# Kernel tuning notes

Hardware: AMD Instinct MI355X
Metric: run time of the kernel (lower is better)

Reference implementation:

```python
import jax, jax.numpy as jnp
import numpy as np

B, T, D_MODEL = 2, 2048, 2048
N_HEADS, N_KV, HEAD_DIM = 16, 8, 128
ROPE_BASE = 10000.0
LAMBDA_INIT = 0.2  # 0.8 - 0.6*exp(-0.3*0), layer_depth=0


def rms_norm(x):
    eps = jnp.finfo(x.dtype).eps
    return x * jax.lax.rsqrt(jnp.mean(x * x, axis=-1, keepdims=True) + eps)


def rope_cos_sin(seq_len, dim):
    inv_freq = 1.0 / (ROPE_BASE ** (np.arange(0, dim, 2, dtype=np.float32) / dim))
    t = np.arange(seq_len, dtype=np.float32)
    freqs = np.outer(t, inv_freq)  # [T, dim/2]
    # original caches cos/sin in bfloat16
    cos = jnp.asarray(np.cos(freqs)).astype(jnp.bfloat16).astype(jnp.float32)
    sin = jnp.asarray(np.sin(freqs)).astype(jnp.bfloat16).astype(jnp.float32)
    return cos[None, :, None, :], sin[None, :, None, :]


def apply_rotary(x, cos, sin):
    d = x.shape[-1] // 2
    x1, x2 = x[..., :d], x[..., d:]
    return jnp.concatenate([x1 * cos + x2 * sin, -x1 * sin + x2 * cos], axis=-1)


def causal_attn(q, k, v):
    # q: [B,T,H,Dq], k: [B,S,H,Dq], v: [B,S,H,Dv]
    scale = 1.0 / np.sqrt(q.shape[-1]).astype(np.float32)
    s = jnp.einsum('bthd,bshd->bhts', q, k) * scale
    mask = jnp.tril(jnp.ones((q.shape[1], k.shape[1]), dtype=bool))
    s = jnp.where(mask, s, -jnp.inf)
    p = jax.nn.softmax(s, axis=-1)
    return jnp.einsum('bhts,bshe->bthe', p, v)


def diff_attention(x, Wq, Wk, Wv, lambda_q1, lambda_k1, lambda_q2, lambda_k2, softmax_scaler):
    b, t, _ = x.shape
    q = (x @ Wq.T).reshape(b, t, N_HEADS, HEAD_DIM)
    k = (x @ Wk.T).reshape(b, t, N_KV, HEAD_DIM)
    v = (x @ Wv.T).reshape(b, t, N_KV // 2, 2 * HEAD_DIM)
    cos, sin = rope_cos_sin(t, HEAD_DIM)
    q, k = rms_norm(q), rms_norm(k)
    q, k = apply_rotary(q, cos, sin), apply_rotary(k, cos, sin)
    k = k.reshape(b, t, 2, N_KV // 2, HEAD_DIM)
    k1, k2 = k[:, :, 0], k[:, :, 1]
    # scalable softmax: q *= scaler_h * log(position)
    pos = jnp.arange(1, t + 1, dtype=jnp.float32).reshape(1, t, 1, 1)
    q = softmax_scaler.reshape(1, 1, -1, 1) * jnp.log(pos) * q
    q = q.reshape(b, t, 2, N_HEADS // 2, HEAD_DIM)
    q1, q2 = q[:, :, 0], q[:, :, 1]
    rep = N_HEADS // N_KV  # GQA repeat
    k1 = jnp.repeat(k1, rep, axis=2)
    k2 = jnp.repeat(k2, rep, axis=2)
    vr = jnp.repeat(v, rep, axis=2)
    y1 = causal_attn(q1, k1, vr)
    y2 = causal_attn(q2, k2, vr)
    lam1 = jnp.exp(jnp.sum(lambda_q1 * lambda_k1))
    lam2 = jnp.exp(jnp.sum(lambda_q2 * lambda_k2))
    lam = lam1 - lam2 + LAMBDA_INIT
    return y1 - lam * y2  # [B,T,N_HEADS//2, 2*HEAD_DIM]


def setup_inputs() -> dict:
    key = jax.random.key(0)
    ks = jax.random.split(key, 8)
    return {
        'x': jax.random.normal(ks[0], (B, T, D_MODEL), dtype=jnp.float32),
        'Wq': jax.random.normal(ks[1], (N_HEADS * HEAD_DIM, D_MODEL), dtype=jnp.float32) * 0.02,
        'Wk': jax.random.normal(ks[2], (N_KV * HEAD_DIM, D_MODEL), dtype=jnp.float32) * 0.02,
        'Wv': jax.random.normal(ks[3], (N_KV * HEAD_DIM, D_MODEL), dtype=jnp.float32) * 0.02,
        'lambda_q1': jax.random.normal(ks[4], (HEAD_DIM // 2,), dtype=jnp.float32) * 0.1,
        'lambda_k1': jax.random.normal(ks[5], (HEAD_DIM // 2,), dtype=jnp.float32) * 0.1,
        'lambda_q2': jax.random.normal(ks[6], (HEAD_DIM // 2,), dtype=jnp.float32) * 0.1,
        'lambda_k2': jax.random.normal(ks[7], (HEAD_DIM // 2,), dtype=jnp.float32) * 0.1,
        'softmax_scaler': jnp.ones((N_HEADS,), dtype=jnp.float32),
    }


def reference(x, Wq, Wk, Wv, lambda_q1, lambda_k1, lambda_q2, lambda_k2, softmax_scaler):
    return diff_attention(x, Wq, Wk, Wv, lambda_q1, lambda_k1, lambda_q2, lambda_k2, softmax_scaler)
```

## Files before the change

### kernel.cpp

```cpp
#include <hip/hip_runtime.h>

#define T_SEQ 2048
#define DMODEL 2048
#define BSZ 2
#define MROWS (BSZ * T_SEQ)
#define NQKV 4096
#define NEG_BIG (-1e30f)

typedef __attribute__((ext_vector_type(8))) _Float16 half8;
typedef __attribute__((ext_vector_type(4))) _Float16 half4;
typedef __attribute__((ext_vector_type(4))) float f32x4;

typedef const __attribute__((address_space(1))) unsigned int* gas_ptr;
typedef __attribute__((address_space(3))) unsigned int* las_ptr;
#define GLD16(g, l) __builtin_amdgcn_global_load_lds((gas_ptr)(g), (las_ptr)(l), 16, 0, 0)

__device__ __forceinline__ unsigned short f2bf(float f) {
  unsigned u = __float_as_uint(f);
  unsigned r = (u + 0x7fffu + ((u >> 16) & 1u)) >> 16;
  return (unsigned short)r;
}
__device__ __forceinline__ float bf2f(unsigned short h) {
  return __uint_as_float(((unsigned)h) << 16);
}

__global__ __launch_bounds__(256) void prep(const float* __restrict__ x,
                                            const float* __restrict__ Wq,
                                            const float* __restrict__ Wk,
                                            const float* __restrict__ Wv,
                                            _Float16* __restrict__ xh,
                                            _Float16* __restrict__ wh,
                                            float* __restrict__ cosT,
                                            float* __restrict__ sinT) {
  int bid = blockIdx.x;
  if (bid < 8192) {
    size_t o = ((size_t)(bid & 4095) * 256 + threadIdx.x) * 8;
    const float* src;
    _Float16* dst;
    if (bid < 4096) {
      src = x + o;
      dst = xh + o;
    } else {
      int row = (int)(o >> 11), col = (int)(o & 2047);
      src = ((row < 2048) ? (Wq + (size_t)row * 2048)
            : (row < 3072) ? (Wk + (size_t)(row - 2048) * 2048)
                           : (Wv + (size_t)(row - 3072) * 2048)) + col;
      dst = wh + o;
    }
    float4 v0 = *(const float4*)(src);
    float4 v1 = *(const float4*)(src + 4);
    half8 r;
    r[0] = (_Float16)v0.x; r[1] = (_Float16)v0.y; r[2] = (_Float16)v0.z; r[3] = (_Float16)v0.w;
    r[4] = (_Float16)v1.x; r[5] = (_Float16)v1.y; r[6] = (_Float16)v1.z; r[7] = (_Float16)v1.w;
    *(half8*)(dst) = r;
  } else {
    int t = bid - 8192;
    int i = threadIdx.x;
    if (i < 64) {
      float inv = (float)pow(10000.0, -((double)(2 * i)) / 128.0);
      float fr = (float)t * inv;
      cosT[t * 64 + i] = bf2f(f2bf(cosf(fr)));
      sinT[t * 64 + i] = bf2f(f2bf(sinf(fr)));
    }
  }
}

__global__ __launch_bounds__(256) void gemm_nt(const _Float16* __restrict__ A,
                                               const _Float16* __restrict__ Bw,
                                               _Float16* __restrict__ C) {
  const int K = DMODEL, N = NQKV;
  __shared__ __align__(16) char As[2][128 * 128];
  __shared__ __align__(16) char Bs[2][128 * 128];
  int tid = threadIdx.x;
  int lane = tid & 63, w = tid >> 6;
  int wm = w >> 1, wn = w & 1;
  int l15 = lane & 15, quad = lane >> 4;
  int bm = blockIdx.y, bn = blockIdx.x;

  const char* Aab = (const char*)(A + (size_t)(bm * 128) * K);
  const char* Bab = (const char*)(Bw + (size_t)(bn * 128) * K);
  int srow = lane >> 3;
  int scol = ((lane & 7) ^ srow) << 4;

  auto stage = [&](int t) {
    int buf = t & 1;
    size_t kb = (size_t)t << 7;
#pragma unroll
    for (int g = 0; g < 4; g++) {
      int row = w * 32 + g * 8 + srow;
      GLD16(Aab + (size_t)row * (K * 2) + kb + scol, &As[buf][w * 4096 + g * 1024]);
    }
#pragma unroll
    for (int g = 0; g < 4; g++) {
      int row = w * 32 + g * 8 + srow;
      GLD16(Bab + (size_t)row * (K * 2) + kb + scol, &Bs[buf][w * 4096 + g * 1024]);
    }
  };

  f32x4 acc[4][4];
#pragma unroll
  for (int i = 0; i < 4; i++)
#pragma unroll
    for (int j = 0; j < 4; j++) acc[i][j] = (f32x4){0.f, 0.f, 0.f, 0.f};

  stage(0);
  for (int t = 0; t < 32; t++) {
    if (t < 31) {
      stage(t + 1);
      asm volatile("s_waitcnt vmcnt(8)" ::: "memory");
    } else {
      asm volatile("s_waitcnt vmcnt(0)" ::: "memory");
    }
    __builtin_amdgcn_s_barrier();
    __builtin_amdgcn_sched_barrier(0);

    const char* ab = As[t & 1];
    const char* bb = Bs[t & 1];
#pragma unroll
    for (int kc = 0; kc < 2; kc++) {
      half8 af[4], bfr[4];
#pragma unroll
      for (int i = 0; i < 4; i++) {
        int row = wm * 64 + i * 16 + l15;
        af[i] = *(const half8*)(ab + row * 128 + ((kc * 64 + quad * 16) ^ ((row & 7) << 4)));
      }
#pragma unroll
      for (int j = 0; j < 4; j++) {
        int row = wn * 64 + j * 16 + l15;
        bfr[j] = *(const half8*)(bb + row * 128 + ((kc * 64 + quad * 16) ^ ((row & 7) << 4)));
      }
#pragma unroll
      for (int i = 0; i < 4; i++)
#pragma unroll
        for (int j = 0; j < 4; j++)
          acc[i][j] = __builtin_amdgcn_mfma_f32_16x16x32_f16(af[i], bfr[j], acc[i][j], 0, 0, 0);
    }

    asm volatile("s_waitcnt lgkmcnt(0)" ::: "memory");
    __builtin_amdgcn_s_barrier();
    __builtin_amdgcn_sched_barrier(0);
  }

#pragma unroll
  for (int i = 0; i < 4; i++)
#pragma unroll
    for (int j = 0; j < 4; j++)
#pragma unroll
      for (int r = 0; r < 4; r++) {
        int row = bm * 128 + wm * 64 + i * 16 + quad * 4 + r;
        int col = bn * 128 + wn * 64 + j * 16 + l15;
        C[(size_t)row * N + col] = (_Float16)acc[i][j][r];
      }
}

__global__ __launch_bounds__(256) void mid(_Float16* __restrict__ qkv,
                                           const float* __restrict__ cosT,
                                           const float* __restrict__ sinT,
                                           _Float16* __restrict__ kp,
                                           _Float16* __restrict__ vt) {
  __shared__ _Float16 tile[32][33];
  int bid = blockIdx.x;
  if (bid < 6144) {
    int tid = threadIdx.x, lane = tid & 63, w = tid >> 6;
    int h = bid >> 8;
    int tkn = (bid & 255) * 16 + w * 4 + (lane >> 4);
    int b = tkn >> 11, t = tkn & 2047;
    int l15 = lane & 15;
    int col0 = (h < 16) ? (h * 128) : (2048 + (h - 16) * 128);
    size_t base = (size_t)tkn * NQKV + col0 + l15 * 8;

    half8 v = *(const half8*)(qkv + base);
    float xf[8];
    float ss = 0.f;
#pragma unroll
    for (int j = 0; j < 8; j++) { xf[j] = (float)v[j]; ss += xf[j] * xf[j]; }
    ss += __shfl_xor(ss, 1, 64);
    ss += __shfl_xor(ss, 2, 64);
    ss += __shfl_xor(ss, 4, 64);
    ss += __shfl_xor(ss, 8, 64);
    float rn = rsqrtf(ss * (1.0f / 128.0f) + 1.1920929e-7f);

    const float* cb = cosT + t * 64 + (lane & 7) * 8;
    const float* sb = sinT + t * 64 + (lane & 7) * 8;
    float4 c0 = *(const float4*)cb, c1 = *(const float4*)(cb + 4);
    float4 s0 = *(const float4*)sb, s1 = *(const float4*)(sb + 4);
    float cc[8] = {c0.x, c0.y, c0.z, c0.w, c1.x, c1.y, c1.z, c1.w};
    float sn[8] = {s0.x, s0.y, s0.z, s0.w, s1.x, s1.y, s1.z, s1.w};
    float sgn = (lane & 8) ? -1.f : 1.f;

    half8 o;
#pragma unroll
    for (int j = 0; j < 8; j++) {
      float xn = xf[j] * rn;
      float xp = __shfl_xor(xn, 8, 64);
      o[j] = (_Float16)(xn * cc[j] + sgn * xp * sn[j]);
    }
    if (h < 16)
      *(half8*)(qkv + base) = o;
    else
      *(half8*)(kp + (((size_t)(b * 8 + (h - 16))) * T_SEQ + t) * 128 + l15 * 8) = o;
  } else {
    int tb = bid - 6144;
    int t0 = (tb & 63) * 32, d0 = ((tb >> 6) & 7) * 32;
    int bz = tb >> 9;
    int b = bz >> 2, vh = bz & 3;
    int tx = threadIdx.x & 31, ty = threadIdx.x >> 5;
#pragma unroll
    for (int i = 0; i < 4; i++) {
      int t = t0 + ty + i * 8;
      tile[ty + i * 8][tx] = qkv[((size_t)(b * T_SEQ + t)) * NQKV + 3072 + vh * 256 + d0 + tx];
    }
    __syncthreads();
#pragma unroll
    for (int i = 0; i < 4; i++) {
      int d = d0 + ty + i * 8;
      vt[(((size_t)(b * 4 + vh)) * 256 + d) * T_SEQ + t0 + tx] = tile[tx][ty + i * 8];
    }
  }
}

__global__ __launch_bounds__(256) void attn(const _Float16* __restrict__ qkv,
                                            const _Float16* __restrict__ kp,
                                            const _Float16* __restrict__ vt,
                                            const float* __restrict__ scaler,
                                            float* __restrict__ y1out,
                                            _Float16* __restrict__ y2out) {
  __shared__ __align__(16) char Ks[2][64 * 256];
  __shared__ __align__(16) char Vs[2][128 * 128];
  __shared__ _Float16 Pt[4 * 16 * 72];

  int tid = threadIdx.x, lane = tid & 63, w = tid >> 6;
  int l15 = lane & 15, quad = lane >> 4;
  int bx = blockIdx.x, hh = blockIdx.y, z = blockIdx.z;
  int b = z >> 1, br = z & 1;
  int qh = br * 8 + hh;
  int kh = br * 4 + (hh >> 1);
  int vh = hh >> 1;

  const char* kbase_b = (const char*)(kp + ((size_t)(b * 8 + kh)) * T_SEQ * 128);
  const char* vbase_b = (const char*)(vt + ((size_t)(b * 4 + vh)) * 256 * T_SEQ);
  _Float16* pw = &Pt[w * 16 * 72];
  float sc = scaler[qh] * 0.08838834764831844f;

  int krow_l = lane >> 4;
  int kpc    = (lane & 15) << 4;
  int vrow_l = lane >> 3;
  int vpc    = (lane & 7) << 4;

  auto stageK = [&](int kt1) {
    int ksr = kt1 * 64;
    char* dstb = Ks[kt1 & 1];
#pragma unroll
    for (int c2 = 0; c2 < 4; c2++) {
      int cc = w * 4 + c2;
      int row = cc * 4 + krow_l;
      const char* src = kbase_b + (((size_t)(ksr + row)) << 8) + (kpc ^ ((row & 7) << 4));
      GLD16(src, dstb + (cc << 10));
    }
  };
  auto stageV = [&](int kt1) {
    int ksb = kt1 * 128;
#pragma unroll
    for (int h = 0; h < 2; h++)
#pragma unroll
      for (int c2 = 0; c2 < 4; c2++) {
        int cc = w * 4 + c2;
        int d = h * 128 + cc * 8 + vrow_l;
        const char* src = vbase_b + (size_t)d * (T_SEQ * 2) + ksb + (vpc ^ (vrow_l << 4));
        GLD16(src, Vs[h] + (cc << 10));
      }
  };

  for (int half = 0; half < 2; half++) {
    int qt = half ? (31 - bx) : bx;
    int t0 = qt * 64;
    int tg = t0 + w * 16 + l15;

    const _Float16* qbase = qkv + ((size_t)(b * T_SEQ + tg)) * NQKV + qh * 128;
    half8 qf[4];
#pragma unroll
    for (int kc = 0; kc < 4; kc++)
      qf[kc] = *(const half8*)(qbase + kc * 32 + quad * 8);

    stageK(0);
    stageV(0);
    __builtin_amdgcn_sched_barrier(0);

    float mrow = NEG_BIG, lrow = 0.f;
    float rowscale = sc * logf((float)(tg + 1)) * 1.44269504f;
    f32x4 acc[16];
#pragma unroll
    for (int nb = 0; nb < 16; nb++) acc[nb] = (f32x4){0.f, 0.f, 0.f, 0.f};

    for (int kt = 0; kt <= qt; kt++) {
      int ks = kt * 64;
      bool notlast = (kt < qt);

      asm volatile("s_waitcnt vmcnt(8)" ::: "memory");
      __builtin_amdgcn_s_barrier();
      __builtin_amdgcn_sched_barrier(0);
      if (notlast) stageK(kt + 1);

      const char* kbuf = Ks[kt & 1];
      f32x4 sv[4];
#pragma unroll
      for (int j = 0; j < 4; j++) {
        int row = j * 16 + l15;
        int sw = (row & 7) << 4;
        const char* kr = kbuf + (row << 8);
        half8 kf0 = *(const half8*)(kr + (((quad << 4) + 0) ^ sw));
        half8 kf1 = *(const half8*)(kr + (((quad << 4) + 64) ^ sw));
        half8 kf2 = *(const half8*)(kr + (((quad << 4) + 128) ^ sw));
        half8 kf3 = *(const half8*)(kr + (((quad << 4) + 192) ^ sw));
        f32x4 a = (f32x4){0.f, 0.f, 0.f, 0.f};
        a = __builtin_amdgcn_mfma_f32_16x16x32_f16(kf0, qf[0], a, 0, 0, 0);
        a = __builtin_amdgcn_mfma_f32_16x16x32_f16(kf1, qf[1], a, 0, 0, 0);
        a = __builtin_amdgcn_mfma_f32_16x16x32_f16(kf2, qf[2], a, 0, 0, 0);
        a = __builtin_amdgcn_mfma_f32_16x16x32_f16(kf3, qf[3], a, 0, 0, 0);
        sv[j] = a;
      }

      bool diag = (kt == qt);
      float s_r[16];
      float mx = NEG_BIG;
#pragma unroll
      for (int j = 0; j < 4; j++)
#pragma unroll
        for (int r = 0; r < 4; r++) {
          float s = sv[j][r] * rowscale;
          if (diag) {
            int kg = ks + j * 16 + quad * 4 + r;
            if (kg > tg) s = NEG_BIG;
          }
          s_r[j * 4 + r] = s;
          mx = fmaxf(mx, s);
        }
      mx = fmaxf(mx, __shfl_xor(mx, 16, 64));
      mx = fmaxf(mx, __shfl_xor(mx, 32, 64));
      float mnew = fmaxf(mrow, mx);
      float alpha = __builtin_amdgcn_exp2f(mrow - mnew);
      float p[16];
      float rs = 0.f;
#pragma unroll
      for (int i = 0; i < 16; i++) {
        p[i] = __builtin_amdgcn_exp2f(s_r[i] - mnew);
        rs += p[i];
      }
      rs += __shfl_xor(rs, 16, 64);
      rs += __shfl_xor(rs, 32, 64);
      lrow = lrow * alpha + rs;
      mrow = mnew;
#pragma unroll
      for (int nb = 0; nb < 16; nb++)
#pragma unroll
        for (int r = 0; r < 4; r++) acc[nb][r] *= alpha;

#pragma unroll
      for (int j = 0; j < 4; j++) {
        half4 pk;
        pk[0] = (_Float16)p[j * 4 + 0];
        pk[1] = (_Float16)p[j * 4 + 1];
        pk[2] = (_Float16)p[j * 4 + 2];
        pk[3] = (_Float16)p[j * 4 + 3];
        *(half4*)&pw[l15 * 72 + j * 16 + quad * 4] = pk;
      }
      half8 pf0 = *(const half8*)&pw[l15 * 72 + quad * 8];
      half8 pf1 = *(const half8*)&pw[l15 * 72 + 32 + quad * 8];

      if (notlast)
        asm volatile("s_waitcnt vmcnt(4)" ::: "memory");
      else
        asm volatile("s_waitcnt vmcnt(0)" ::: "memory");
      __builtin_amdgcn_s_barrier();
      __builtin_amdgcn_sched_barrier(0);

#pragma unroll
      for (int h = 0; h < 2; h++) {
#pragma unroll
        for (int nbl = 0; nbl < 8; nbl++) {
          int row = nbl * 16 + l15;
          int sw = (row & 7) << 4;
          const char* vr = Vs[h] + (row << 7);
          half8 vf0 = *(const half8*)(vr + (((quad << 4) + 0) ^ sw));
          half8 vf1 = *(const half8*)(vr + (((quad << 4) + 64) ^ sw));
          int nb = h * 8 + nbl;
          acc[nb] = __builtin_amdgcn_mfma_f32_16x16x32_f16(vf0, pf0, acc[nb], 0, 0, 0);
          acc[nb] = __builtin_amdgcn_mfma_f32_16x16x32_f16(vf1, pf1, acc[nb], 0, 0, 0);
        }
      }

      asm volatile("s_waitcnt lgkmcnt(0)" ::: "memory");
      __builtin_amdgcn_s_barrier();
      __builtin_amdgcn_sched_barrier(0);
      if (notlast) stageV(kt + 1);
    }

    float linv = 1.0f / lrow;
    size_t base = ((size_t)(b * T_SEQ + tg)) * 2048 + hh * 256 + quad * 4;
    if (br) {
#pragma unroll
      for (int nb = 0; nb < 16; nb++) {
        half4 hv;
        hv[0] = (_Float16)(acc[nb][0] * linv);
        hv[1] = (_Float16)(acc[nb][1] * linv);
        hv[2] = (_Float16)(acc[nb][2] * linv);
        hv[3] = (_Float16)(acc[nb][3] * linv);
        *(half4*)(y2out + base + nb * 16) = hv;
      }
    } else {
#pragma unroll
      for (int nb = 0; nb < 16; nb++) {
        float4 fv;
        fv.x = acc[nb][0] * linv;
        fv.y = acc[nb][1] * linv;
        fv.z = acc[nb][2] * linv;
        fv.w = acc[nb][3] * linv;
        *(float4*)(y1out + base + nb * 16) = fv;
      }
    }
  }
}

__global__ __launch_bounds__(256) void combine(float* __restrict__ out,
                                               const _Float16* __restrict__ y2,
                                               const float* __restrict__ lq1,
                                               const float* __restrict__ lk1,
                                               const float* __restrict__ lq2,
                                               const float* __restrict__ lk2) {
  int lane = threadIdx.x & 63;
  float a = lq1[lane] * lk1[lane];
  float bb = lq2[lane] * lk2[lane];
#pragma unroll
  for (int m = 1; m < 64; m <<= 1) {
    a += __shfl_xor(a, m, 64);
    bb += __shfl_xor(bb, m, 64);
  }
  float lam = expf(a) - expf(bb) + 0.2f;

  size_t o = ((size_t)blockIdx.x * 256 + threadIdx.x) * 8;
  half8 yv = *(const half8*)(y2 + o);
  float4 a0 = *(float4*)(out + o);
  float4 a1 = *(float4*)(out + o + 4);
  a0.x -= lam * (float)yv[0];
  a0.y -= lam * (float)yv[1];
  a0.z -= lam * (float)yv[2];
  a0.w -= lam * (float)yv[3];
  a1.x -= lam * (float)yv[4];
  a1.y -= lam * (float)yv[5];
  a1.z -= lam * (float)yv[6];
  a1.w -= lam * (float)yv[7];
  *(float4*)(out + o) = a0;
  *(float4*)(out + o + 4) = a1;
}

extern "C" void kernel_launch(void* const* d_in, const int* in_sizes, int n_in,
                              void* d_out, int out_size, void* d_ws, size_t ws_size,
                              hipStream_t stream) {
  const float* x   = (const float*)d_in[0];
  const float* Wq  = (const float*)d_in[1];
  const float* Wk  = (const float*)d_in[2];
  const float* Wv  = (const float*)d_in[3];
  const float* lq1 = (const float*)d_in[4];
  const float* lk1 = (const float*)d_in[5];
  const float* lq2 = (const float*)d_in[6];
  const float* lk2 = (const float*)d_in[7];
  const float* scaler = (const float*)d_in[8];
  float* out = (float*)d_out;

  char* W = (char*)d_ws;
  _Float16* xh   = (_Float16*)(W + 0);
  _Float16* wh   = (_Float16*)(W + 16777216);
  _Float16* qkvh = (_Float16*)(W + 33554432);
  _Float16* kph  = (_Float16*)(W + 0);
  _Float16* vtb  = (_Float16*)(W + 8388608);
  _Float16* y2h  = (_Float16*)(W + 16777216);
  float* cosT    = out;
  float* sinT    = out + 131072;

  prep<<<10240, 256, 0, stream>>>(x, Wq, Wk, Wv, xh, wh, cosT, sinT);
  gemm_nt<<<dim3(NQKV / 128, MROWS / 128), 256, 0, stream>>>(xh, wh, qkvh);
  mid<<<10240, 256, 0, stream>>>(qkvh, cosT, sinT, kph, vtb);
  attn<<<dim3(16, 8, BSZ * 2), 256, 0, stream>>>(qkvh, kph, vtb, scaler, out, y2h);
  combine<<<4096, 256, 0, stream>>>(out, y2h, lq1, lk1, lq2, lk2);
}
```

Baseline: 313.5 us.

## Enlarge QKV GEMM to 256x256 tiles with 8 waves and interleaved scheduling

The QKV projection GEMM moves from 128x128 tiles with 4 waves to 256x256 tiles with 8 waves. Each wave now computes a 128x64 sub-tile, with LDS reads interleaved against MFMA batches under barriers and s_setprio hints, and the next k-tile prefetch is issued mid-iteration. This raises operand reuse per LDS byte and cuts global traffic. The cost is 128KB of LDS, more accumulator registers, and only 256 blocks, which is about one wave of work on 256 CUs.

After: 314.3 us. No clear change (+0.3%).

```diff
diff --git a/kernel.cpp b/kernel.cpp
--- a/kernel.cpp
+++ b/kernel.cpp
@@ -65,91 +65,124 @@
   }
 }
 
-__global__ __launch_bounds__(256) void gemm_nt(const _Float16* __restrict__ A,
+__global__ __launch_bounds__(512) void gemm_nt(const _Float16* __restrict__ A,
                                                const _Float16* __restrict__ Bw,
                                                _Float16* __restrict__ C) {
   const int K = DMODEL, N = NQKV;
-  __shared__ __align__(16) char As[2][128 * 128];
-  __shared__ __align__(16) char Bs[2][128 * 128];
+  __shared__ __align__(16) char As[2][2][16384];
+  __shared__ __align__(16) char Bs[2][2][16384];
   int tid = threadIdx.x;
   int lane = tid & 63, w = tid >> 6;
-  int wm = w >> 1, wn = w & 1;
+  int wr = w >> 2, wc = w & 3;
+  int cb = wc & 1, bh = wc >> 1;
   int l15 = lane & 15, quad = lane >> 4;
   int bm = blockIdx.y, bn = blockIdx.x;
 
-  const char* Aab = (const char*)(A + (size_t)(bm * 128) * K);
-  const char* Bab = (const char*)(Bw + (size_t)(bn * 128) * K);
-  int srow = lane >> 3;
-  int scol = ((lane & 7) ^ srow) << 4;
+  const char* Aab = (const char*)(A + (size_t)(bm * 256) * K);
+  const char* Bab = (const char*)(Bw + (size_t)(bn * 256) * K);
+  int scol = ((lane & 7) ^ (lane >> 3)) << 4;
 
   auto stage = [&](int t) {
-    int buf = t & 1;
-    size_t kb = (size_t)t << 7;
-#pragma unroll
-    for (int g = 0; g < 4; g++) {
-      int row = w * 32 + g * 8 + srow;
-      GLD16(Aab + (size_t)row * (K * 2) + kb + scol, &As[buf][w * 4096 + g * 1024]);
-    }
-#pragma unroll
-    for (int g = 0; g < 4; g++) {
-      int row = w * 32 + g * 8 + srow;
-      GLD16(Bab + (size_t)row * (K * 2) + kb + scol, &Bs[buf][w * 4096 + g * 1024]);
+    int bt = t & 1;
+    int kb = t * 128;
+#pragma unroll
+    for (int g = 0; g < 8; g++) {
+      int mtx = g >> 2;
+      int h   = (g >> 1) & 1;
+      int j   = g & 1;
+      int row = h * 128 + w * 16 + j * 8 + (lane >> 3);
+      const char* src = (mtx ? Bab : Aab) + (size_t)row * (K * 2) + kb + scol;
+      char* dst = (mtx ? &Bs[bt][h][0] : &As[bt][h][0]) + (w * 16 + j * 8) * 128;
+      GLD16(src, dst);
     }
   };
 
-  f32x4 acc[4][4];
-#pragma unroll
-  for (int i = 0; i < 4; i++)
+  f32x4 acc[8][4];
+#pragma unroll
+  for (int i = 0; i < 8; i++)
 #pragma unroll
     for (int j = 0; j < 4; j++) acc[i][j] = (f32x4){0.f, 0.f, 0.f, 0.f};
 
   stage(0);
+  asm volatile("s_waitcnt vmcnt(0)" ::: "memory");
+  __builtin_amdgcn_s_barrier();
+  __builtin_amdgcn_sched_barrier(0);
+
   for (int t = 0; t < 32; t++) {
-    if (t < 31) {
-      stage(t + 1);
-      asm volatile("s_waitcnt vmcnt(8)" ::: "memory");
-    } else {
-      asm volatile("s_waitcnt vmcnt(0)" ::: "memory");
-    }
-    __builtin_amdgcn_s_barrier();
-    __builtin_amdgcn_sched_barrier(0);
-
-    const char* ab = As[t & 1];
-    const char* bb = Bs[t & 1];
-#pragma unroll
-    for (int kc = 0; kc < 2; kc++) {
-      half8 af[4], bfr[4];
-#pragma unroll
-      for (int i = 0; i < 4; i++) {
-        int row = wm * 64 + i * 16 + l15;
-        af[i] = *(const half8*)(ab + row * 128 + ((kc * 64 + quad * 16) ^ ((row & 7) << 4)));
-      }
-#pragma unroll
-      for (int j = 0; j < 4; j++) {
-        int row = wn * 64 + j * 16 + l15;
-        bfr[j] = *(const half8*)(bb + row * 128 + ((kc * 64 + quad * 16) ^ ((row & 7) << 4)));
-      }
-#pragma unroll
-      for (int i = 0; i < 4; i++)
-#pragma unroll
-        for (int j = 0; j < 4; j++)
-          acc[i][j] = __builtin_amdgcn_mfma_f32_16x16x32_f16(af[i], bfr[j], acc[i][j], 0, 0, 0);
-    }
-
-    asm volatile("s_waitcnt lgkmcnt(0)" ::: "memory");
-    __builtin_amdgcn_s_barrier();
-    __builtin_amdgcn_sched_barrier(0);
-  }
-
-#pragma unroll
-  for (int i = 0; i < 4; i++)
-#pragma unroll
-    for (int j = 0; j < 4; j++)
+    const char* Ahb = &As[t & 1][wr][0];
+    const char* Bhb = &Bs[t & 1][bh][0];
+    half8 af[4], bf[4];
+
+#define RD_A(FB, KST)                                                              \
+  {                                                                                \
+    _Pragma("unroll") for (int fr = 0; fr < 4; fr++) {                             \
+      int row = ((FB) + fr) * 16 + l15;                                            \
+      af[fr] = *(const half8*)(Ahb + row * 128 +                                   \
+                               (((KST)*64 + quad * 16) ^ ((l15 & 7) << 4)));       \
+    }                                                                              \
+  }
+#define RD_B(KST)                                                                  \
+  {                                                                                \
+    _Pragma("unroll") for (int fc = 0; fc < 4; fc++) {                             \
+      int row = cb * 64 + fc * 16 + l15;                                           \
+      bf[fc] = *(const half8*)(Bhb + row * 128 +                                   \
+                               (((KST)*64 + quad * 16) ^ ((l15 & 7) << 4)));       \
+    }                                                                              \
+  }
+#define MM(FB)                                                                     \
+  {                                                                                \
+    _Pragma("unroll") for (int fr = 0; fr < 4; fr++)                               \
+        _Pragma("unroll") for (int fc = 0; fc < 4; fc++)                           \
+            acc[(FB) + fr][fc] = __builtin_amdgcn_mfma_f32_16x16x32_f16(           \
+                af[fr], bf[fc], acc[(FB) + fr][fc], 0, 0, 0);                      \
+  }
+#define BAR()                       \
+  __builtin_amdgcn_s_barrier();     \
+  __builtin_amdgcn_sched_barrier(0);
+
+    RD_A(0, 0);
+    RD_B(0);
+    if (t < 31) stage(t + 1);
+    BAR();
+    __builtin_amdgcn_s_setprio(1);
+    MM(0);
+    __builtin_amdgcn_s_setprio(0);
+    BAR();
+    RD_A(4, 0);
+    BAR();
+    __builtin_amdgcn_s_setprio(1);
+    MM(4);
+    __builtin_amdgcn_s_setprio(0);
+    BAR();
+    RD_A(0, 1);
+    RD_B(1);
+    BAR();
+    __builtin_amdgcn_s_setprio(1);
+    MM(0);
+    __builtin_amdgcn_s_setprio(0);
+    BAR();
+    RD_A(4, 1);
+    BAR();
+    __builtin_amdgcn_s_setprio(1);
+    MM(4);
+    __builtin_amdgcn_s_setprio(0);
+    asm volatile("s_waitcnt vmcnt(0)" ::: "memory");
+    BAR();
+#undef RD_A
+#undef RD_B
+#undef MM
+#undef BAR
+  }
+
+#pragma unroll
+  for (int FR = 0; FR < 8; FR++)
+#pragma unroll
+    for (int fc = 0; fc < 4; fc++)
 #pragma unroll
       for (int r = 0; r < 4; r++) {
-        int row = bm * 128 + wm * 64 + i * 16 + quad * 4 + r;
-        int col = bn * 128 + wn * 64 + j * 16 + l15;
-        C[(size_t)row * N + col] = (_Float16)acc[i][j][r];
+        int row = bm * 256 + wr * 128 + FR * 16 + quad * 4 + r;
+        int col = bn * 256 + wc * 64 + fc * 16 + l15;
+        C[(size_t)row * N + col] = (_Float16)acc[FR][fc][r];
       }
 }
 
@@ -478,7 +511,7 @@
   float* sinT    = out + 131072;
 
   prep<<<10240, 256, 0, stream>>>(x, Wq, Wk, Wv, xh, wh, cosT, sinT);
-  gemm_nt<<<dim3(NQKV / 128, MROWS / 128), 256, 0, stream>>>(xh, wh, qkvh);
+  gemm_nt<<<dim3(NQKV / 256, MROWS / 256), 512, 0, stream>>>(xh, wh, qkvh);
   mid<<<10240, 256, 0, stream>>>(qkvh, cosT, sinT, kph, vtb);
   attn<<<dim3(16, 8, BSZ * 2), 256, 0, stream>>>(qkvh, kph, vtb, scaler, out, y2h);
   combine<<<4096, 256, 0, stream>>>(out, y2h, lq1, lk1, lq2, lk2);
```
